# Kernel tuning notes

Hardware: AMD Instinct MI355X
Metric: run time of the kernel (lower is better)

## Reference

```python
import jax, jax.numpy as jnp
import numpy as np

S, D, H = 2048, 1024, 16
DH = D // H
EPS = 1e-5


def setup_inputs() -> dict:
    key = jax.random.key(0)
    ks = jax.random.split(key, 6)
    scale = 0.02
    return {
        "inputs": jax.random.normal(ks[0], (S, D), dtype=jnp.float32),
        "ln_w": jnp.ones((D,), dtype=jnp.float32),
        "ln_b": jnp.zeros((D,), dtype=jnp.float32),
        "Wq": jax.random.normal(ks[1], (D, D), dtype=jnp.float32) * scale,
        "Wk": jax.random.normal(ks[2], (D, D), dtype=jnp.float32) * scale,
        "Wv": jax.random.normal(ks[3], (D, D), dtype=jnp.float32) * scale,
        "Wo": jax.random.normal(ks[4], (D, D), dtype=jnp.float32) * scale,
    }


def reference(inputs, ln_w, ln_b, Wq, Wk, Wv, Wo):
    # Pre-LayerNorm (per token), matching eqx.nn.LayerNorm (eps=1e-5)
    mu = jnp.mean(inputs, axis=-1, keepdims=True)
    var = jnp.var(inputs, axis=-1, keepdims=True)
    x = (inputs - mu) / jnp.sqrt(var + EPS) * ln_w + ln_b  # [S, D]

    # QKV projections (eqx Linear: y = W @ x, no bias) -> [S, H, DH]
    q = (x @ Wq.T).reshape(S, H, DH)
    k = (x @ Wk.T).reshape(S, H, DH)
    v = (x @ Wv.T).reshape(S, H, DH)

    # Scaled dot-product attention; softmax forced to full precision
    scores = jnp.einsum("shd,thd->hst", q, k) / jnp.sqrt(jnp.asarray(DH, x.dtype))
    attn = jax.nn.softmax(scores.astype(jnp.float32), axis=-1).astype(x.dtype)
    # (dropout is identity in inference mode)
    ctx = jnp.einsum("hst,thd->shd", attn, v).reshape(S, D)

    out = ctx @ Wo.T  # output projection
    # outer dropout is identity in inference mode; residual add
    return out + inputs
```

## Files before the change

### kernel.cpp

```cpp
#include <hip/hip_runtime.h>
#include <cstdint>
#include <cstddef>

typedef unsigned short u16;
typedef unsigned int u32;
typedef __attribute__((ext_vector_type(8))) short bf16x8;
typedef __attribute__((ext_vector_type(4))) short bf16x4;
typedef __attribute__((ext_vector_type(4))) float f32x4;
typedef __attribute__((ext_vector_type(4))) unsigned short u16x4;

#if __has_builtin(__builtin_amdgcn_mfma_f32_16x16x16bf16_1k)
#define MFMA16(a, b, c) __builtin_amdgcn_mfma_f32_16x16x16bf16_1k(a, b, c, 0, 0, 0)
#else
static __device__ __forceinline__ f32x4 mfma16_asm(bf16x4 a, bf16x4 b, f32x4 c) {
  asm volatile("v_mfma_f32_16x16x16_bf16 %0, %1, %2, %0\n\ts_nop 4"
               : "+v"(c) : "v"(a), "v"(b));
  return c;
}
#define MFMA16(a, b, c) mfma16_asm(a, b, c)
#endif

#if __has_builtin(__builtin_amdgcn_exp2f)
#define EXP2(x) __builtin_amdgcn_exp2f(x)
#else
#define EXP2(x) exp2f(x)
#endif

__device__ __forceinline__ u16 f2b(float f) {
  union { float f; unsigned u; } un; un.f = f;
  unsigned u = un.u;
  return (u16)((u + 0x7fffu + ((u >> 16) & 1u)) >> 16);
}

__device__ __forceinline__ u32 pkbf(float a, float b) {
  union { float f; u32 u; } ua, ub; ua.f = a; ub.f = b;
  return ((ua.u + 0x8000u) >> 16) | (((ub.u + 0x8000u) >> 16) << 16);
}

__device__ __forceinline__ void gload_lds16(const u16* g, u16* l) {
  __builtin_amdgcn_global_load_lds(
      (const __attribute__((address_space(1))) void*)g,
      (__attribute__((address_space(3))) void*)l, 16, 0, 0);
}

__device__ __forceinline__ void gemm128x128(
    const u16* __restrict__ A, const u16* __restrict__ B,
    u16* smA, u16* smB, int bm, int bn,
    float* outf, u16* outb, const float* __restrict__ resid, int ostride)
{
  const int tid = threadIdx.x;
  const int wave = tid >> 6, lane = tid & 63;
  const int quad = lane >> 4, l16 = lane & 15;
  const int wm = wave >> 1, wn = wave & 1;

  f32x4 acc[4][4];
  const f32x4 zero4 = {0.f, 0.f, 0.f, 0.f};
#pragma unroll
  for (int i = 0; i < 4; i++)
#pragma unroll
    for (int j = 0; j < 4; j++) acc[i][j] = zero4;

  const u16* Ab = A + (size_t)(bm * 128) * 1024;
  const u16* Bb = B + (size_t)(bn * 128) * 1024;

#define PSTAGE(buf, k0)                                                          \
  {                                                                              \
    _Pragma("unroll")                                                            \
    for (int i = 0; i < 4; i++) {                                                \
      const int idx = i * 256 + tid;                                             \
      const int row = idx >> 3, sl = idx & 7;                                    \
      const int g = (sl ^ (row & 7)) * 8;                                        \
      gload_lds16(Ab + (size_t)row * 1024 + (k0) + g,                            \
                  smA + (buf) * 8192 + (size_t)(i * 256 + wave * 64) * 8);       \
      gload_lds16(Bb + (size_t)row * 1024 + (k0) + g,                            \
                  smB + (buf) * 8192 + (size_t)(i * 256 + wave * 64) * 8);       \
    }                                                                            \
  }

  PSTAGE(0, 0);
  __syncthreads();
  for (int t = 0; t < 16; t++) {
    const int cur = t & 1;
    if (t < 15) PSTAGE(cur ^ 1, (t + 1) * 64);
    const u16* sa = smA + cur * 8192;
    const u16* sb = smB + cur * 8192;
#pragma unroll
    for (int ks = 0; ks < 2; ks++) {
      const int swz = ((ks * 4 + quad) ^ (l16 & 7)) * 8;
      bf16x8 afr[4], bfr[4];
#pragma unroll
      for (int mt = 0; mt < 4; mt++)
        afr[mt] = *(const bf16x8*)(sa + (wm * 64 + mt * 16 + l16) * 64 + swz);
#pragma unroll
      for (int nt = 0; nt < 4; nt++)
        bfr[nt] = *(const bf16x8*)(sb + (wn * 64 + nt * 16 + l16) * 64 + swz);
#pragma unroll
      for (int mt = 0; mt < 4; mt++)
#pragma unroll
        for (int nt = 0; nt < 4; nt++)
          acc[mt][nt] = __builtin_amdgcn_mfma_f32_16x16x32_bf16(afr[mt], bfr[nt], acc[mt][nt], 0, 0, 0);
    }
    __syncthreads();
  }
#undef PSTAGE

#pragma unroll
  for (int mt = 0; mt < 4; mt++)
#pragma unroll
    for (int nt = 0; nt < 4; nt++)
#pragma unroll
      for (int r = 0; r < 4; r++) {
        const int row = bm * 128 + wm * 64 + mt * 16 + quad * 4 + r;
        const int col = bn * 128 + wn * 64 + nt * 16 + l16;
        if (outb) outb[(size_t)row * ostride + col] = f2b(acc[mt][nt][r]);
        else outf[(size_t)row * ostride + col] =
                 acc[mt][nt][r] + resid[(size_t)row * ostride + col];
      }
}

__global__ __launch_bounds__(256, 2) void proj_k(
    const u16* __restrict__ xb, const u16* __restrict__ Wb,
    u16* __restrict__ qkbuf, u16* __restrict__ vTb)
{
  __shared__ u16 smA[2 * 128 * 64];
  __shared__ u16 smB[2 * 128 * 64];
  int b = blockIdx.x;
  const u16 *A, *B; u16* o; int bm, bn;
  if (b < 256) {
    const int c = b & 7, i = b >> 3;
    bm = ((c >> 2) << 3) | (i & 7);
    bn = ((c & 3) << 2) | (i >> 3);
    A = xb; B = Wb; o = qkbuf;
  } else {
    b -= 256;
    const int c = b & 7, i = b >> 3;
    bm = i & 7;
    bn = (c << 1) | (i >> 3);
    A = Wb + (size_t)2 * (1 << 20); B = xb; o = vTb;
  }
  gemm128x128(A, B, smA, smB, bm, bn, nullptr, o, nullptr, 2048);
}

__global__ __launch_bounds__(256, 2) void out_k(
    const u16* __restrict__ ctxb, const u16* __restrict__ Wob,
    float* __restrict__ out, const float* __restrict__ x)
{
  __shared__ u16 smA[2 * 128 * 64];
  __shared__ u16 smB[2 * 128 * 64];
  const int b = blockIdx.x;
  const int c = b & 7, i = b >> 3;
  const int bm = ((c >> 2) << 3) | (i & 7);
  const int bn = ((c & 3) << 1) | (i >> 3);
  gemm128x128(ctxb, Wob, smA, smB, bm, bn, out, nullptr, x, 1024);
}

__global__ __launch_bounds__(256) void pre_k(
    const float* __restrict__ x, const float* __restrict__ lnw, const float* __restrict__ lnb,
    const float* __restrict__ w0, const float* __restrict__ w1,
    const float* __restrict__ w2, const float* __restrict__ w3,
    u16* __restrict__ xb, u16* __restrict__ Wb)
{
  const int b = blockIdx.x;
  const int tid = threadIdx.x;
  if (b < 2048) {
    const int s = b;
    const float4 v = ((const float4*)(x + (size_t)s * 1024))[tid];
    float sum = v.x + v.y + v.z + v.w;
    float sq  = v.x * v.x + v.y * v.y + v.z * v.z + v.w * v.w;
#pragma unroll
    for (int off = 32; off >= 1; off >>= 1) {
      sum += __shfl_down(sum, off);
      sq  += __shfl_down(sq, off);
    }
    __shared__ float sS[4], sQ[4];
    const int wave = tid >> 6, lane = tid & 63;
    if (lane == 0) { sS[wave] = sum; sQ[wave] = sq; }
    __syncthreads();
    const float ts = sS[0] + sS[1] + sS[2] + sS[3];
    const float tq = sQ[0] + sQ[1] + sQ[2] + sQ[3];
    const float mu = ts * (1.0f / 1024.0f);
    const float var = tq * (1.0f / 1024.0f) - mu * mu;
    const float rstd = rsqrtf(var + 1e-5f);
    const float4 wv = ((const float4*)lnw)[tid];
    const float4 bv = ((const float4*)lnb)[tid];
    u16x4 o;
    o[0] = f2b((v.x - mu) * rstd * wv.x + bv.x);
    o[1] = f2b((v.y - mu) * rstd * wv.y + bv.y);
    o[2] = f2b((v.z - mu) * rstd * wv.z + bv.z);
    o[3] = f2b((v.w - mu) * rstd * wv.w + bv.w);
    *(u16x4*)(xb + (size_t)s * 1024 + tid * 4) = o;
  } else {
    const unsigned i = (unsigned)(b - 2048) * 1024u + tid * 4u;
    const unsigned NW = 1u << 20;
    const float* src; unsigned loc; float sc;
    if (i < NW)            { src = w0; loc = i;           sc = 0.18033688f; }
    else if (i < 2u * NW)  { src = w1; loc = i - NW;      sc = 1.0f; }
    else if (i < 3u * NW)  { src = w2; loc = i - 2u * NW; sc = 1.0f; }
    else                   { src = w3; loc = i - 3u * NW; sc = 1.0f; }
    const float4 v = *(const float4*)(src + loc);
    u16x4 r;
    r[0] = f2b(v.x * sc); r[1] = f2b(v.y * sc); r[2] = f2b(v.z * sc); r[3] = f2b(v.w * sc);
    *(u16x4*)(Wb + i) = r;
  }
}

__global__ __launch_bounds__(256, 3) void attn_k(
    const u16* __restrict__ qkbuf,
    const u16* __restrict__ vT,
    u16* __restrict__ ctx)
{
  const int bid = blockIdx.x;
  const int work = (bid & 7) * 64 + (bid >> 3);
  const int h = work >> 5;
  const int q0 = (work & 31) * 64;
  __shared__ __align__(16) float arena[4 * 64 * 32];
  const int tid = threadIdx.x;
  const int wave = tid >> 6, lane = tid & 63;
  const int quad = lane >> 4, l16 = lane & 15;

  bf16x8 qf[4][2];
#pragma unroll
  for (int s = 0; s < 4; s++)
#pragma unroll
    for (int ks = 0; ks < 2; ks++)
      qf[s][ks] = *(const bf16x8*)(qkbuf + (size_t)(q0 + s * 16 + l16) * 2048 + h * 64 + ks * 32 + quad * 8);

  const f32x4 zero4 = {0.f, 0.f, 0.f, 0.f};
  f32x4 Oacc[4][4];
#pragma unroll
  for (int s = 0; s < 4; s++)
#pragma unroll
    for (int dt = 0; dt < 4; dt++) Oacc[s][dt] = zero4;
  float lacc[4] = {0.f, 0.f, 0.f, 0.f};

  const u16* kb = qkbuf + 1024 + h * 64 + (size_t)(wave * 32 + l16) * 2048;
  const u16* vb = vT + (size_t)(h * 64 + l16) * 2048 + wave * 32;

  for (int T = 0; T < 16; T++) {
    f32x4 st[2][4];
#pragma unroll
    for (int ntl = 0; ntl < 2; ntl++) {
      const u16* kr = kb + (size_t)(T * 128 + ntl * 16) * 2048;
      const bf16x8 ka0 = *(const bf16x8*)(kr + quad * 8);
      const bf16x8 ka1 = *(const bf16x8*)(kr + 32 + quad * 8);
#pragma unroll
      for (int s = 0; s < 4; s++) {
        f32x4 t0 = __builtin_amdgcn_mfma_f32_16x16x32_bf16(ka0, qf[s][0], zero4, 0, 0, 0);
        st[ntl][s] = __builtin_amdgcn_mfma_f32_16x16x32_bf16(ka1, qf[s][1], t0, 0, 0, 0);
      }
    }

    bf16x4 pk[2][4];
#pragma unroll
    for (int ntl = 0; ntl < 2; ntl++)
#pragma unroll
      for (int s = 0; s < 4; s++) {
        const float p0 = EXP2(st[ntl][s][0]);
        const float p1 = EXP2(st[ntl][s][1]);
        const float p2 = EXP2(st[ntl][s][2]);
        const float p3 = EXP2(st[ntl][s][3]);
        lacc[s] += (p0 + p1) + (p2 + p3);
        union { u32 u[2]; bf16x4 v; } pp;
        pp.u[0] = pkbf(p0, p1);
        pp.u[1] = pkbf(p2, p3);
        pk[ntl][s] = pp.v;
      }

#pragma unroll
    for (int ntl = 0; ntl < 2; ntl++)
#pragma unroll
      for (int dt = 0; dt < 4; dt++) {
        const bf16x4 bv = *(const bf16x4*)(vb + (size_t)(dt * 16) * 2048 + T * 128 + ntl * 16 + quad * 4);
#pragma unroll
        for (int s = 0; s < 4; s++)
          Oacc[s][dt] = MFMA16(pk[ntl][s], bv, Oacc[s][dt]);
      }
  }

  float* rl = arena;
#pragma unroll
  for (int s = 0; s < 4; s++) {
    float l = lacc[s];
    l += __shfl_xor(l, 16);
    l += __shfl_xor(l, 32);
    if (quad == 0) rl[wave * 64 + s * 16 + l16] = l;
  }
  __syncthreads();
  const int m = tid >> 2;
  const int c8 = (tid & 3) * 8;
  const float inv = 1.0f / (rl[m] + rl[64 + m] + rl[128 + m] + rl[192 + m]);
  __syncthreads();

  float* ro = arena;
  const int msw3 = (m & 3) << 3;
#pragma unroll
  for (int pass = 0; pass < 2; pass++) {
#pragma unroll
    for (int s = 0; s < 4; s++)
#pragma unroll
      for (int dtl = 0; dtl < 2; dtl++)
#pragma unroll
        for (int r = 0; r < 4; r++) {
          const int mr = s * 16 + quad * 4 + r;
          const int dc = (dtl * 16 + l16) ^ ((mr & 3) << 3);
          ro[wave * 2048 + mr * 32 + dc] = Oacc[s][pass * 2 + dtl][r];
        }
    __syncthreads();
    u16* dst = ctx + (size_t)(q0 + m) * 1024 + h * 64 + pass * 32 + c8;
    float v[8];
#pragma unroll
    for (int j = 0; j < 8; j++) {
      const int base = m * 32 + ((c8 + j) ^ msw3);
      v[j] = ro[base] + ro[2048 + base] + ro[4096 + base] + ro[6144 + base];
    }
    u16x4 o0, o1;
#pragma unroll
    for (int j = 0; j < 4; j++) { o0[j] = f2b(v[j] * inv); o1[j] = f2b(v[4 + j] * inv); }
    *(u16x4*)dst = o0;
    *(u16x4*)(dst + 4) = o1;
    __syncthreads();
  }
}

extern "C" void kernel_launch(void* const* d_in, const int* in_sizes, int n_in,
                              void* d_out, int out_size, void* d_ws, size_t ws_size,
                              hipStream_t stream)
{
  const float* x   = (const float*)d_in[0];
  const float* lnw = (const float*)d_in[1];
  const float* lnb = (const float*)d_in[2];
  const float* Wq  = (const float*)d_in[3];
  const float* Wk  = (const float*)d_in[4];
  const float* Wv  = (const float*)d_in[5];
  const float* Wo  = (const float*)d_in[6];

  u16* ws    = (u16*)d_ws;
  u16* xb    = ws;
  u16* Wb    = xb + (size_t)2048 * 1024;
  u16* qkbuf = Wb + (size_t)4 * 1024 * 1024;
  u16* vTb   = qkbuf + (size_t)2048 * 2048;
  u16* ctxb  = vTb + (size_t)1024 * 2048;

  pre_k<<<6144, 256, 0, stream>>>(x, lnw, lnb, Wq, Wk, Wv, Wo, xb, Wb);
  proj_k<<<384, 256, 0, stream>>>(xb, Wb, qkbuf, vTb);
  attn_k<<<512, 256, 0, stream>>>(qkbuf, vTb, ctxb);
  out_k<<<128, 256, 0, stream>>>(ctxb, Wb + (size_t)3 * (1 << 20), (float*)d_out, x);
}
```

Before: 173.6 us.

## Stage K/V tiles through double-buffered LDS with async global-to-LDS loads

The attention kernel previously had each wave read its own K and V fragments straight from global memory every iteration. Now all four waves cooperatively stage 64-key K and V tiles into swizzled, double-buffered LDS with global_load_lds, prefetching the next tile while computing the current one behind explicit vmcnt waits and barriers. MFMA sections are wrapped in s_setprio, and the final cross-wave reduction switches to a new swizzle that allows vectorized float4 LDS reads. This adds two barriers per iteration and doubles the iteration count, trading synchronization cost for shared, overlapped loads.

```diff
diff --git a/kernel.cpp b/kernel.cpp
--- a/kernel.cpp
+++ b/kernel.cpp
@@ -25,6 +25,9 @@
 #else
 #define EXP2(x) exp2f(x)
 #endif
+
+#define WAITV(N) asm volatile("s_waitcnt vmcnt(" #N ")" ::: "memory")
+#define MEMFENCE() asm volatile("" ::: "memory")
 
 __device__ __forceinline__ u16 f2b(float f) {
   union { float f; unsigned u; } un; un.f = f;
@@ -213,10 +216,13 @@
   const int work = (bid & 7) * 64 + (bid >> 3);
   const int h = work >> 5;
   const int q0 = (work & 31) * 64;
-  __shared__ __align__(16) float arena[4 * 64 * 32];
+  __shared__ __align__(16) float arena[8192];
+  u16* kvbuf = (u16*)arena;
   const int tid = threadIdx.x;
   const int wave = tid >> 6, lane = tid & 63;
   const int quad = lane >> 4, l16 = lane & 15;
+  const int a7 = l16 & 7;
+  const u16* kg = qkbuf + 1024 + h * 64;
 
   bf16x8 qf[4][2];
 #pragma unroll
@@ -233,49 +239,73 @@
     for (int dt = 0; dt < 4; dt++) Oacc[s][dt] = zero4;
   float lacc[4] = {0.f, 0.f, 0.f, 0.f};
 
-  const u16* kb = qkbuf + 1024 + h * 64 + (size_t)(wave * 32 + l16) * 2048;
-  const u16* vb = vT + (size_t)(h * 64 + l16) * 2048 + wave * 32;
-
-  for (int T = 0; T < 16; T++) {
-    f32x4 st[2][4];
-#pragma unroll
-    for (int ntl = 0; ntl < 2; ntl++) {
-      const u16* kr = kb + (size_t)(T * 128 + ntl * 16) * 2048;
-      const bf16x8 ka0 = *(const bf16x8*)(kr + quad * 8);
-      const bf16x8 ka1 = *(const bf16x8*)(kr + 32 + quad * 8);
-#pragma unroll
-      for (int s = 0; s < 4; s++) {
-        f32x4 t0 = __builtin_amdgcn_mfma_f32_16x16x32_bf16(ka0, qf[s][0], zero4, 0, 0, 0);
-        st[ntl][s] = __builtin_amdgcn_mfma_f32_16x16x32_bf16(ka1, qf[s][1], t0, 0, 0, 0);
-      }
-    }
-
-    bf16x4 pk[2][4];
-#pragma unroll
-    for (int ntl = 0; ntl < 2; ntl++)
-#pragma unroll
-      for (int s = 0; s < 4; s++) {
-        const float p0 = EXP2(st[ntl][s][0]);
-        const float p1 = EXP2(st[ntl][s][1]);
-        const float p2 = EXP2(st[ntl][s][2]);
-        const float p3 = EXP2(st[ntl][s][3]);
-        lacc[s] += (p0 + p1) + (p2 + p3);
-        union { u32 u[2]; bf16x4 v; } pp;
-        pp.u[0] = pkbf(p0, p1);
-        pp.u[1] = pkbf(p2, p3);
-        pk[ntl][s] = pp.v;
-      }
-
-#pragma unroll
-    for (int ntl = 0; ntl < 2; ntl++)
-#pragma unroll
-      for (int dt = 0; dt < 4; dt++) {
-        const bf16x4 bv = *(const bf16x4*)(vb + (size_t)(dt * 16) * 2048 + T * 128 + ntl * 16 + quad * 4);
-#pragma unroll
-        for (int s = 0; s < 4; s++)
-          Oacc[s][dt] = MFMA16(pk[ntl][s], bv, Oacc[s][dt]);
-      }
-  }
+#define STAGE(T, bf)                                                                     \
+  {                                                                                      \
+    _Pragma("unroll")                                                                    \
+    for (int i = 0; i < 2; i++) {                                                        \
+      const int idx = (wave * 2 + i) * 64 + lane;                                        \
+      const int row = idx >> 3, sl = (idx & 7) ^ (row & 7);                              \
+      gload_lds16(kg + (size_t)((T) * 64 + row) * 2048 + sl * 8,                         \
+                  kvbuf + (bf) * 8192 + (size_t)((wave * 2 + i) * 64) * 8);              \
+      gload_lds16(vT + (size_t)(h * 64 + row) * 2048 + (T) * 64 + sl * 8,                \
+                  kvbuf + (bf) * 8192 + 4096 + (size_t)((wave * 2 + i) * 64) * 8);       \
+    }                                                                                    \
+  }
+
+  STAGE(0, 0);
+
+  for (int T = 0; T < 32; T++) {
+    const int bf = T & 1;
+    if (T + 1 < 32) {
+      STAGE(T + 1, 1 - bf);
+      WAITV(4);
+    } else {
+      WAITV(0);
+    }
+    __builtin_amdgcn_s_barrier();
+    const u16* kb = kvbuf + bf * 8192;
+    const u16* vb = kb + 4096;
+
+    const u16* kr = kb + (wave * 16 + l16) * 64;
+    const bf16x8 ka0 = *(const bf16x8*)(kr + ((quad ^ a7) * 8));
+    const bf16x8 ka1 = *(const bf16x8*)(kr + (((4 + quad) ^ a7) * 8));
+    f32x4 st[4];
+    __builtin_amdgcn_s_setprio(1);
+#pragma unroll
+    for (int s = 0; s < 4; s++) {
+      f32x4 t0 = __builtin_amdgcn_mfma_f32_16x16x32_bf16(ka0, qf[s][0], zero4, 0, 0, 0);
+      st[s] = __builtin_amdgcn_mfma_f32_16x16x32_bf16(ka1, qf[s][1], t0, 0, 0, 0);
+    }
+    __builtin_amdgcn_s_setprio(0);
+
+    bf16x4 pk[4];
+#pragma unroll
+    for (int s = 0; s < 4; s++) {
+      const float p0 = EXP2(st[s][0]);
+      const float p1 = EXP2(st[s][1]);
+      const float p2 = EXP2(st[s][2]);
+      const float p3 = EXP2(st[s][3]);
+      lacc[s] += (p0 + p1) + (p2 + p3);
+      union { u32 u[2]; bf16x4 v; } pp;
+      pp.u[0] = pkbf(p0, p1);
+      pp.u[1] = pkbf(p2, p3);
+      pk[s] = pp.v;
+    }
+
+#pragma unroll
+    for (int dt = 0; dt < 4; dt++) {
+      const bf16x4 bv = *(const bf16x4*)(vb + (dt * 16 + l16) * 64 +
+          (((wave * 2 + (quad >> 1)) ^ a7) * 8 + (quad & 1) * 4));
+      __builtin_amdgcn_s_setprio(1);
+#pragma unroll
+      for (int s = 0; s < 4; s++)
+        Oacc[s][dt] = MFMA16(pk[s], bv, Oacc[s][dt]);
+      __builtin_amdgcn_s_setprio(0);
+    }
+    MEMFENCE();
+    __builtin_amdgcn_s_barrier();
+  }
+#undef STAGE
 
   float* rl = arena;
 #pragma unroll
@@ -292,7 +322,7 @@
   __syncthreads();
 
   float* ro = arena;
-  const int msw3 = (m & 3) << 3;
+  const int fl = ((m >> 2) & 1) << 4;
 #pragma unroll
   for (int pass = 0; pass < 2; pass++) {
 #pragma unroll
@@ -302,20 +332,25 @@
 #pragma unroll
         for (int r = 0; r < 4; r++) {
           const int mr = s * 16 + quad * 4 + r;
-          const int dc = (dtl * 16 + l16) ^ ((mr & 3) << 3);
+          const int dc = (dtl * 16 + l16) ^ ((quad & 1) << 4);
           ro[wave * 2048 + mr * 32 + dc] = Oacc[s][pass * 2 + dtl][r];
         }
     __syncthreads();
     u16* dst = ctx + (size_t)(q0 + m) * 1024 + h * 64 + pass * 32 + c8;
-    float v[8];
-#pragma unroll
-    for (int j = 0; j < 8; j++) {
-      const int base = m * 32 + ((c8 + j) ^ msw3);
-      v[j] = ro[base] + ro[2048 + base] + ro[4096 + base] + ro[6144 + base];
+    float v8[8];
+#pragma unroll
+    for (int j4 = 0; j4 < 2; j4++) {
+      const int base = m * 32 + ((c8 + j4 * 4) ^ fl);
+      const f32x4 a0 = *(const f32x4*)&ro[base];
+      const f32x4 a1 = *(const f32x4*)&ro[2048 + base];
+      const f32x4 a2 = *(const f32x4*)&ro[4096 + base];
+      const f32x4 a3 = *(const f32x4*)&ro[6144 + base];
+#pragma unroll
+      for (int j = 0; j < 4; j++) v8[j4 * 4 + j] = a0[j] + a1[j] + a2[j] + a3[j];
     }
     u16x4 o0, o1;
 #pragma unroll
-    for (int j = 0; j < 4; j++) { o0[j] = f2b(v[j] * inv); o1[j] = f2b(v[4 + j] * inv); }
+    for (int j = 0; j < 4; j++) { o0[j] = f2b(v8[j] * inv); o1[j] = f2b(v8[4 + j] * inv); }
     *(u16x4*)dst = o0;
     *(u16x4*)(dst + 4) = o1;
     __syncthreads();
```

Result: faster. 153.2 us (-11.8%).
